# Optimization experiments

Measured on AMD Instinct MI355X. Metric: run time of the kernel, lower is better.

Reference implementation:

```python
import jax, jax.numpy as jnp
import numpy as np

MARKET_DIM, VELOCITY_DIM, AGENT_STATE_DIM = 20, 10, 10
RUNNER_DIM, POSITION_DIM, MAX_RUNNERS = 24, 8, 30
RUNNER_INPUT_DIM = RUNNER_DIM + POSITION_DIM            # 32
MARKET_TOTAL_DIM = MARKET_DIM + VELOCITY_DIM + AGENT_STATE_DIM  # 40
OBS_DIM = MARKET_DIM + VELOCITY_DIM + MAX_RUNNERS * RUNNER_DIM + AGENT_STATE_DIM + MAX_RUNNERS * POSITION_DIM  # 1000
TD_IDX = MARKET_DIM + (VELOCITY_DIM - 4)                # 26
B, T = 256, 64
MLP_H, LSTM_H = 128, 256
LSTM_IN = MLP_H + 2 * MLP_H                             # 384


def setup_inputs() -> dict:
    key = jax.random.key(0)
    ks = jax.random.split(key, 32)

    def w(k, o, i):
        return (jax.random.normal(k, (o, i), jnp.float32) / np.sqrt(i)).astype(jnp.float32)

    z = lambda n: jnp.zeros((n,), jnp.float32)
    return dict(
        obs=jax.random.normal(ks[0], (B, T, OBS_DIM), jnp.float32),
        # runner encoder: 32 -> 128 -> 128 -> 128
        re_w0=w(ks[1], MLP_H, RUNNER_INPUT_DIM), re_b0=z(MLP_H),
        re_w1=w(ks[2], MLP_H, MLP_H), re_b1=z(MLP_H),
        re_w2=w(ks[3], MLP_H, MLP_H), re_b2=z(MLP_H),
        # market encoder: 40 -> 128 -> 128 -> 128
        me_w0=w(ks[4], MLP_H, MARKET_TOTAL_DIM), me_b0=z(MLP_H),
        me_w1=w(ks[5], MLP_H, MLP_H), me_b1=z(MLP_H),
        me_w2=w(ks[6], MLP_H, MLP_H), me_b2=z(MLP_H),
        # TimeLSTM cell (single layer)
        W_ih=w(ks[7], 4 * LSTM_H, LSTM_IN), b_ih=z(4 * LSTM_H),
        W_hh=w(ks[8], 4 * LSTM_H, LSTM_H),
        W_dt=jnp.zeros((LSTM_H,), jnp.float32),
        # actor head: 384 -> 128 -> 2
        a_w0=w(ks[9], MLP_H, MLP_H + LSTM_H), a_b0=z(MLP_H),
        a_w1=w(ks[10], 2, MLP_H) * 0.01, a_b1=z(2),
        # critic head: 256 -> 128 -> 1
        c_w0=w(ks[11], MLP_H, LSTM_H), c_b0=z(MLP_H),
        c_w1=w(ks[12], 1, MLP_H), c_b1=z(1),
        log_std=jnp.zeros((MAX_RUNNERS * 2,), jnp.float32),
    )


def _mlp3(x, w0, b0, w1, b1, w2, b2):
    x = jax.nn.relu(x @ w0.T + b0)
    x = jax.nn.relu(x @ w1.T + b1)
    return x @ w2.T + b2


def _mlp2(x, w0, b0, w1, b1):
    return jax.nn.relu(x @ w0.T + b0) @ w1.T + b1


def reference(obs,
              re_w0, re_b0, re_w1, re_b1, re_w2, re_b2,
              me_w0, me_b0, me_w1, me_b1, me_w2, me_b2,
              W_ih, b_ih, W_hh, W_dt,
              a_w0, a_b0, a_w1, a_b1,
              c_w0, c_b0, c_w1, c_b1,
              log_std):
    b, t, _ = obs.shape
    of = obs.reshape(b * t, -1)
    market = of[:, :MARKET_DIM]
    vel = of[:, MARKET_DIM:MARKET_DIM + VELOCITY_DIM]
    rs = MARKET_DIM + VELOCITY_DIM
    re_ = rs + MAX_RUNNERS * RUNNER_DIM
    runners = of[:, rs:re_].reshape(b * t, MAX_RUNNERS, RUNNER_DIM)
    agent = of[:, re_:re_ + AGENT_STATE_DIM]
    ps = re_ + AGENT_STATE_DIM
    pos = of[:, ps:ps + MAX_RUNNERS * POSITION_DIM].reshape(b * t, MAX_RUNNERS, POSITION_DIM)

    market_feats = jnp.concatenate([market, vel, agent], axis=-1)        # (BT, 40)
    runner_feats = jnp.concatenate([runners, pos], axis=-1)              # (BT, R, 32)

    market_emb = _mlp3(market_feats, me_w0, me_b0, me_w1, me_b1, me_w2, me_b2)  # (BT, 128)
    runner_embs = _mlp3(runner_feats, re_w0, re_b0, re_w1, re_b1, re_w2, re_b2)  # (BT, R, 128)
    r_mean = runner_embs.mean(axis=1)
    r_max = runner_embs.max(axis=1)

    lstm_in = jnp.concatenate([market_emb, r_mean, r_max], axis=-1).reshape(b, t, LSTM_IN)
    dt = of[:, TD_IDX].reshape(b, t)

    h0 = jnp.zeros((b, LSTM_H), obs.dtype)
    c0 = jnp.zeros_like(h0)

    def step(hc, xs):
        h, c = hc
        x, d = xs                                           # (B, 384), (B,)
        gates = x @ W_ih.T + b_ih + h @ W_hh.T              # (B, 4H)
        i, f, g, o = jnp.split(gates, 4, axis=-1)
        f = f + W_dt * d[:, None]                           # time-modulated forget gate
        i, f, o = jax.nn.sigmoid(i), jax.nn.sigmoid(f), jax.nn.sigmoid(o)
        g = jnp.tanh(g)
        c_new = f * c + i * g
        h_new = o * jnp.tanh(c_new)
        return (h_new, c_new), None

    (h, c), _ = jax.lax.scan(step, (h0, c0), (lstm_in.transpose(1, 0, 2), dt.T))
    lstm_out = h  # layer_norm disabled -> identity

    runner_last = runner_embs.reshape(b, t, MAX_RUNNERS, MLP_H)[:, -1]   # (B, R, 128)
    actor_in = jnp.concatenate(
        [runner_last, jnp.broadcast_to(lstm_out[:, None, :], (b, MAX_RUNNERS, LSTM_H))], axis=-1)
    action_mean = _mlp2(actor_in, a_w0, a_b0, a_w1, a_b1).reshape(b, MAX_RUNNERS * 2)
    action_log_std = jnp.broadcast_to(log_std, action_mean.shape)
    value = _mlp2(lstm_out, c_w0, c_b0, c_w1, c_b1)                      # (B, 1)
    return action_mean, action_log_std, value, h, c
```

## Files before the change

kernel.cpp:

```cpp
#include <hip/hip_runtime.h>
#include <hip/hip_bf16.h>
#include <math.h>

#define Bn 256
#define Tn 64
#define OBSD 1000
#define NR 30
#define HD 128
#define LH 256
#define LIN 384
#define TDI 26

#define AM_OFF 0
#define ALS_OFF 15360
#define V_OFF 30720
#define H_OFF 30976
#define C_OFF 96512

typedef unsigned short u16;
typedef short bf16x8 __attribute__((ext_vector_type(8)));
typedef float f32x4 __attribute__((ext_vector_type(4)));

__device__ __forceinline__ float sigm(float x){ return 1.f/(1.f+__expf(-x)); }
__device__ __forceinline__ float tanhfast(float x){
    float ax = fabsf(x);
    float e = __expf(2.f*ax);
    float t = 1.f - 2.f/(e+1.f);
    return copysignf(t, x);
}

__device__ __forceinline__ u16 f2b(float f){
    union { __hip_bfloat16 h; u16 u; } cv;
    cv.h = __float2bfloat16(f);
    return cv.u;
}

__device__ __forceinline__ bf16x8 ld_b128_sys(const u16* p){
    bf16x8 r;
    asm volatile("global_load_dwordx4 %0, %1, off sc0 sc1"
                 : "=v"(r) : "v"(p) : "memory");
    return r;
}
__device__ __forceinline__ void st_b16_sys(u16* p, unsigned v){
    asm volatile("global_store_short %0, %1, off sc0 sc1"
                 :: "v"(p), "v"(v) : "memory");
}

#define MFMA(a,b,c) __builtin_amdgcn_mfma_f32_16x16x32_bf16(a,b,c,0,0,0)

__global__ void k_pack(const float* __restrict__ src, u16* __restrict__ dst,
                       int N, int K, int Kpad)
{
    int t = blockIdx.x*256 + threadIdx.x;
    if (t >= N*Kpad) return;
    int j = t / Kpad, k = t - j*Kpad;
    float v = (k < K) ? src[j*K + k] : 0.f;
    int ntile = j>>4, jr = j&15, kc = k>>5, ko = k&31;
    int lane = ((ko>>3)<<4) | jr, elem = ko&7;
    int KC = Kpad>>5;
    dst[(size_t)(((ntile*KC + kc)*64) + lane)*8 + elem] = f2b(v);
}

__global__ void k_pack_gi(const float* __restrict__ src, u16* __restrict__ dst, int K)
{
    int KC = K >> 5;
    int t = blockIdx.x*256 + threadIdx.x;
    if (t >= 1024*K) return;
    int n = t / K, k = t - n*K;
    int nt = n>>4, jr = n&15;
    int jg = nt>>2, g = nt&3;
    float v = src[(size_t)(g*256 + jg*16 + jr)*K + k];
    int kc = k>>5, ko = k&31;
    int lane = ((ko>>3)<<4) | jr, e = ko&7;
    dst[(size_t)(((nt*KC + kc)*64) + lane)*8 + e] = f2b(v);
}

__global__ void k_dtv(const float* __restrict__ obs, float* __restrict__ dtv)
{
    int idx = blockIdx.x*256 + threadIdx.x;
    int b = idx >> 6, t = idx & 63;
    dtv[t*256 + b] = obs[(size_t)idx*OBSD + TDI];
}

__global__ __launch_bounds__(256) void k_embed(
    const float* __restrict__ obs,
    const u16* __restrict__ pw0, const float* __restrict__ re_b0,
    const u16* __restrict__ pw1, const float* __restrict__ re_b1,
    const u16* __restrict__ pw2, const float* __restrict__ re_b2,
    u16* __restrict__ li_bf, float* __restrict__ runner_last)
{
    __shared__ __align__(16) u16 xr[64*40];
    __shared__ __align__(16) u16 act1[64*136];
    __shared__ __align__(16) u16 act2[64*136];
    __shared__ float bs0[128], bs1[128], bs2[128];

    int blk = blockIdx.x, tid = threadIdx.x;
    int bt0 = blk*2;

    for (int idx=tid; idx<2048; idx+=256){
        int r = idx>>5, k = idx&31;
        int sb = r>>5, rr = r&31;
        const float* row = obs + (size_t)(bt0+sb)*OBSD;
        float v = 0.f;
        if (rr < 30) v = (k<24) ? row[30 + rr*24 + k] : row[760 + rr*8 + (k-24)];
        xr[r*40 + k] = f2b(v);
    }
    if (tid < 128){ bs0[tid]=re_b0[tid]; bs1[tid]=re_b1[tid]; bs2[tid]=re_b2[tid]; }
    __syncthreads();

    int lane = tid & 63, wv = tid >> 6;
    int lr = lane & 15, lk = lane >> 4;
    f32x4 zero = {0.f,0.f,0.f,0.f};

    f32x4 d[4][2];

    {
        bf16x8 a0[4];
        #pragma unroll
        for (int m=0;m<4;m++) a0[m] = *(const bf16x8*)(xr + (m*16+lr)*40 + lk*8);
        #pragma unroll
        for (int ns=0; ns<2; ns++){
            int n = 2*wv + ns;
            bf16x8 b = *(const bf16x8*)(pw0 + (size_t)(n*64 + lane)*8);
            #pragma unroll
            for (int m=0;m<4;m++) d[m][ns] = MFMA(a0[m], b, zero);
        }
    }
    #pragma unroll
    for (int m=0;m<4;m++)
        #pragma unroll
        for (int ns=0;ns<2;ns++){
            int col = (2*wv+ns)*16 + lr;
            float bias = bs0[col];
            #pragma unroll
            for (int r=0;r<4;r++)
                act1[(m*16+lk*4+r)*136 + col] = f2b(fmaxf(d[m][ns][r] + bias, 0.f));
        }
    __syncthreads();

    #pragma unroll
    for (int m=0;m<4;m++)
        #pragma unroll
        for (int ns=0;ns<2;ns++) d[m][ns] = zero;
    #pragma unroll
    for (int kc=0; kc<4; kc++){
        bf16x8 am[4];
        #pragma unroll
        for (int m=0;m<4;m++) am[m] = *(const bf16x8*)(act1 + (m*16+lr)*136 + kc*32 + lk*8);
        #pragma unroll
        for (int ns=0; ns<2; ns++){
            int n = 2*wv + ns;
            bf16x8 b = *(const bf16x8*)(pw1 + (size_t)((n*4 + kc)*64 + lane)*8);
            #pragma unroll
            for (int m=0;m<4;m++) d[m][ns] = MFMA(am[m], b, d[m][ns]);
        }
    }
    #pragma unroll
    for (int m=0;m<4;m++)
        #pragma unroll
        for (int ns=0;ns<2;ns++){
            int col = (2*wv+ns)*16 + lr;
            float bias = bs1[col];
            #pragma unroll
            for (int r=0;r<4;r++)
                act2[(m*16+lk*4+r)*136 + col] = f2b(fmaxf(d[m][ns][r] + bias, 0.f));
        }
    __syncthreads();

    #pragma unroll
    for (int m=0;m<4;m++)
        #pragma unroll
        for (int ns=0;ns<2;ns++) d[m][ns] = zero;
    #pragma unroll
    for (int kc=0; kc<4; kc++){
        bf16x8 am[4];
        #pragma unroll
        for (int m=0;m<4;m++) am[m] = *(const bf16x8*)(act2 + (m*16+lr)*136 + kc*32 + lk*8);
        #pragma unroll
        for (int ns=0; ns<2; ns++){
            int n = 2*wv + ns;
            bf16x8 b = *(const bf16x8*)(pw2 + (size_t)((n*4 + kc)*64 + lane)*8);
            #pragma unroll
            for (int m=0;m<4;m++) d[m][ns] = MFMA(am[m], b, d[m][ns]);
        }
    }

    u16* li0 = li_bf + (size_t)bt0*LIN;
    u16* li1 = li_bf + (size_t)(bt0+1)*LIN;
    bool last1 = (((bt0+1) & 63) == 63);
    int bb1 = (bt0+1) >> 6;

    #pragma unroll
    for (int ns=0; ns<2; ns++){
        int col = (2*wv+ns)*16 + lr;
        float bias = bs2[col];
        float vals[4][4];
        float s0=0.f, m0=-3.4e38f, s1=0.f, m1=-3.4e38f;
        #pragma unroll
        for (int m=0;m<4;m++)
            #pragma unroll
            for (int r=0;r<4;r++){
                int rw = m*16 + lk*4 + r;
                float v = d[m][ns][r] + bias;
                vals[m][r] = v;
                if (m < 2){
                    bool ok = rw < 30;
                    s0 += ok ? v : 0.f;
                    m0 = fmaxf(m0, ok ? v : -3.4e38f);
                } else {
                    bool ok = (rw-32) < 30;
                    s1 += ok ? v : 0.f;
                    m1 = fmaxf(m1, ok ? v : -3.4e38f);
                }
            }
        s0 += __shfl_xor(s0, 16); s0 += __shfl_xor(s0, 32);
        m0 = fmaxf(m0, __shfl_xor(m0, 16)); m0 = fmaxf(m0, __shfl_xor(m0, 32));
        s1 += __shfl_xor(s1, 16); s1 += __shfl_xor(s1, 32);
        m1 = fmaxf(m1, __shfl_xor(m1, 16)); m1 = fmaxf(m1, __shfl_xor(m1, 32));
        if (lk == 0){
            li0[128 + col] = f2b(s0 * (1.0f/30.0f));
            li0[256 + col] = f2b(m0);
        }
        if (lk == 1){
            li1[128 + col] = f2b(s1 * (1.0f/30.0f));
            li1[256 + col] = f2b(m1);
        }
        if (last1){
            #pragma unroll
            for (int m=2;m<4;m++)
                #pragma unroll
                for (int r=0;r<4;r++){
                    int rw = m*16 + lk*4 + r - 32;
                    if (rw < 30) runner_last[(size_t)bb1*3840 + rw*128 + col] = vals[m][r];
                }
        }
    }
}

__global__ __launch_bounds__(256) void k_market(
    const float* __restrict__ obs,
    const u16* __restrict__ pm0, const float* __restrict__ me_b0,
    const u16* __restrict__ pm1, const float* __restrict__ me_b1,
    const u16* __restrict__ pm2, const float* __restrict__ me_b2,
    u16* __restrict__ li_bf)
{
    __shared__ __align__(16) u16 xm[32*72];
    __shared__ __align__(16) u16 ma1[32*136];
    __shared__ __align__(16) u16 ma2[32*136];
    __shared__ float bs0[128], bs1[128], bs2[128];

    int bt0 = blockIdx.x*32, tid = threadIdx.x;
    for (int idx=tid; idx<2048; idx+=256){
        int r = idx>>6, k = idx&63;
        const float* row = obs + (size_t)(bt0+r)*OBSD;
        float v = 0.f;
        if (k < 30) v = row[k];
        else if (k < 40) v = row[720 + k];
        xm[r*72 + k] = f2b(v);
    }
    if (tid < 128){ bs0[tid]=me_b0[tid]; bs1[tid]=me_b1[tid]; bs2[tid]=me_b2[tid]; }
    __syncthreads();

    int lane = tid & 63, wv = tid >> 6;
    int lr = lane & 15, lk = lane >> 4;
    f32x4 zero = {0.f,0.f,0.f,0.f};
    f32x4 d[2][2];

    #pragma unroll
    for (int m=0;m<2;m++)
        #pragma unroll
        for (int ns=0;ns<2;ns++) d[m][ns] = zero;
    #pragma unroll
    for (int kc=0; kc<2; kc++){
        bf16x8 a0 = *(const bf16x8*)(xm + lr*72      + kc*32 + lk*8);
        bf16x8 a1 = *(const bf16x8*)(xm + (16+lr)*72 + kc*32 + lk*8);
        #pragma unroll
        for (int ns=0; ns<2; ns++){
            int n = 2*wv + ns;
            bf16x8 b = *(const bf16x8*)(pm0 + (size_t)((n*2 + kc)*64 + lane)*8);
            d[0][ns] = MFMA(a0, b, d[0][ns]);
            d[1][ns] = MFMA(a1, b, d[1][ns]);
        }
    }
    #pragma unroll
    for (int m=0;m<2;m++)
        #pragma unroll
        for (int ns=0;ns<2;ns++){
            int col = (2*wv+ns)*16 + lr;
            float bias = bs0[col];
            #pragma unroll
            for (int r=0;r<4;r++){
                int rw = m*16 + lk*4 + r;
                ma1[rw*136 + col] = f2b(fmaxf(d[m][ns][r] + bias, 0.f));
            }
        }
    __syncthreads();

    #pragma unroll
    for (int m=0;m<2;m++)
        #pragma unroll
        for (int ns=0;ns<2;ns++) d[m][ns] = zero;
    #pragma unroll
    for (int kc=0; kc<4; kc++){
        bf16x8 a0 = *(const bf16x8*)(ma1 + lr*136      + kc*32 + lk*8);
        bf16x8 a1 = *(const bf16x8*)(ma1 + (16+lr)*136 + kc*32 + lk*8);
        #pragma unroll
        for (int ns=0; ns<2; ns++){
            int n = 2*wv + ns;
            bf16x8 b = *(const bf16x8*)(pm1 + (size_t)((n*4 + kc)*64 + lane)*8);
            d[0][ns] = MFMA(a0, b, d[0][ns]);
            d[1][ns] = MFMA(a1, b, d[1][ns]);
        }
    }
    #pragma unroll
    for (int m=0;m<2;m++)
        #pragma unroll
        for (int ns=0;ns<2;ns++){
            int col = (2*wv+ns)*16 + lr;
            float bias = bs1[col];
            #pragma unroll
            for (int r=0;r<4;r++){
                int rw = m*16 + lk*4 + r;
                ma2[rw*136 + col] = f2b(fmaxf(d[m][ns][r] + bias, 0.f));
            }
        }
    __syncthreads();

    #pragma unroll
    for (int m=0;m<2;m++)
        #pragma unroll
        for (int ns=0;ns<2;ns++) d[m][ns] = zero;
    #pragma unroll
    for (int kc=0; kc<4; kc++){
        bf16x8 a0 = *(const bf16x8*)(ma2 + lr*136      + kc*32 + lk*8);
        bf16x8 a1 = *(const bf16x8*)(ma2 + (16+lr)*136 + kc*32 + lk*8);
        #pragma unroll
        for (int ns=0; ns<2; ns++){
            int n = 2*wv + ns;
            bf16x8 b = *(const bf16x8*)(pm2 + (size_t)((n*4 + kc)*64 + lane)*8);
            d[0][ns] = MFMA(a0, b, d[0][ns]);
            d[1][ns] = MFMA(a1, b, d[1][ns]);
        }
    }
    #pragma unroll
    for (int m=0;m<2;m++)
        #pragma unroll
        for (int ns=0;ns<2;ns++){
            int col = (2*wv+ns)*16 + lr;
            float bias = bs2[col];
            #pragma unroll
            for (int r=0;r<4;r++){
                int rw = m*16 + lk*4 + r;
                li_bf[(size_t)(bt0+rw)*LIN + col] = f2b(d[m][ns][r] + bias);
            }
        }
}

__global__ __launch_bounds__(256) void k_xw(
    const u16* __restrict__ A, const u16* __restrict__ pwih,
    const float* __restrict__ b_ih, float* __restrict__ xw)
{
    __shared__ __align__(16) u16 bsh[48*512];

    int tid = threadIdx.x;
    int lane = tid & 63, wv = tid >> 6;
    int lr = lane & 15, lk = lane >> 4;
    int r0 = blockIdx.x*128 + wv*32;

    bf16x8 a[2][12];
    #pragma unroll
    for (int m=0;m<2;m++)
        #pragma unroll
        for (int kc=0;kc<12;kc++)
            a[m][kc] = *(const bf16x8*)(A + (size_t)(r0+m*16+lr)*384 + kc*32 + lk*8);

    for (int jg=0; jg<16; jg++){
        {
            const bf16x8* src = (const bf16x8*)(pwih + (size_t)jg*48*512);
            bf16x8* dst = (bf16x8*)bsh;
            #pragma unroll
            for (int i=0;i<12;i++)
                dst[tid + i*256] = src[tid + i*256];
        }
        __syncthreads();

        f32x4 acc[2][4];
        #pragma unroll
        for (int g=0; g<4; g++){
            float bias = b_ih[g*256 + jg*16 + lr];
            f32x4 v = {bias,bias,bias,bias};
            acc[0][g]=v; acc[1][g]=v;
        }
        #pragma unroll
        for (int kc=0; kc<12; kc++){
            bf16x8 b0 = *(const bf16x8*)(bsh + (size_t)((0*12+kc)*64+lane)*8);
            bf16x8 b1 = *(const bf16x8*)(bsh + (size_t)((1*12+kc)*64+lane)*8);
            bf16x8 b2 = *(const bf16x8*)(bsh + (size_t)((2*12+kc)*64+lane)*8);
            bf16x8 b3 = *(const bf16x8*)(bsh + (size_t)((3*12+kc)*64+lane)*8);
            #pragma unroll
            for (int m=0;m<2;m++){
                acc[m][0] = MFMA(a[m][kc], b0, acc[m][0]);
                acc[m][1] = MFMA(a[m][kc], b1, acc[m][1]);
                acc[m][2] = MFMA(a[m][kc], b2, acc[m][2]);
                acc[m][3] = MFMA(a[m][kc], b3, acc[m][3]);
            }
        }
        #pragma unroll
        for (int m=0;m<2;m++)
            #pragma unroll
            for (int g=0;g<4;g++)
                #pragma unroll
                for (int r=0;r<4;r++)
                    xw[(size_t)(r0+m*16+lk*4+r)*1024 + (jg*4+g)*16 + lr] = acc[m][g][r];
        __syncthreads();
    }
}

__global__ __launch_bounds__(256,1) void k_lstm_pair(
    const float* __restrict__ xw, const u16* __restrict__ pwhh,
    const float* __restrict__ W_dt, const float* __restrict__ dtv,
    u16* __restrict__ hb0, u16* __restrict__ hb1,
    float* __restrict__ hout, float* __restrict__ cout,
    unsigned int* __restrict__ flags)
{
    int tid = threadIdx.x;
    int lane = tid & 63, wv = tid >> 6;
    int lr = lane & 15, lk = lane >> 4;
    int blk = blockIdx.x;
    int p = blk >> 1, hf = blk & 1;
    int bb0 = p*16;
    int jg0 = hf*8 + wv*2;

    bf16x8 bfr[2][4][8];
    #pragma unroll
    for (int jl=0;jl<2;jl++)
        #pragma unroll
        for (int g=0;g<4;g++)
            #pragma unroll
            for (int kc=0;kc<8;kc++)
                bfr[jl][g][kc] = *(const bf16x8*)(pwhh + (size_t)((((jg0+jl)*4+g)*8+kc)*64+lane)*8);

    float wdt0 = W_dt[jg0*16 + lr];
    float wdt1 = W_dt[(jg0+1)*16 + lr];

    float cst[2][4] = {{0.f,0.f,0.f,0.f},{0.f,0.f,0.f,0.f}};
    bf16x8 a[8];
    #pragma unroll
    for (int kc=0;kc<8;kc++) a[kc] = (bf16x8)(short)0;

    int bth = bb0 + lk*4;

    float xwn[2][4][4];
    #pragma unroll
    for (int jl=0;jl<2;jl++)
        #pragma unroll
        for (int g=0;g<4;g++)
            #pragma unroll
            for (int r=0;r<4;r++)
                xwn[jl][g][r] = xw[(size_t)((bth+r)*64)*1024 + ((jg0+jl)*4+g)*16 + lr];
    float4 dtn = *(const float4*)(dtv + bth);

    unsigned int* myflag   = &flags[blk*64];
    unsigned int* partflag = &flags[(blk^1)*64];

    for (int t=0; t<64; t++){
        asm volatile("s_waitcnt vmcnt(0)" ::: "memory");
        __builtin_amdgcn_sched_barrier(0);

        f32x4 acc[2][4];
        #pragma unroll
        for (int jl=0;jl<2;jl++)
            #pragma unroll
            for (int g=0;g<4;g++){
                f32x4 v;
                v[0]=xwn[jl][g][0]; v[1]=xwn[jl][g][1];
                v[2]=xwn[jl][g][2]; v[3]=xwn[jl][g][3];
                acc[jl][g] = v;
            }

        #pragma unroll
        for (int kc=0; kc<8; kc++){
            #pragma unroll
            for (int jl=0;jl<2;jl++){
                acc[jl][0] = MFMA(a[kc], bfr[jl][0][kc], acc[jl][0]);
                acc[jl][1] = MFMA(a[kc], bfr[jl][1][kc], acc[jl][1]);
                acc[jl][2] = MFMA(a[kc], bfr[jl][2][kc], acc[jl][2]);
                acc[jl][3] = MFMA(a[kc], bfr[jl][3][kc], acc[jl][3]);
            }
        }

        u16* hw = (t&1) ? hb1 : hb0;
        #pragma unroll
        for (int jl=0;jl<2;jl++){
            float wdt = jl ? wdt1 : wdt0;
            int jcol = (jg0+jl)*16 + lr;
            #pragma unroll
            for (int r=0;r<4;r++){
                float dd = (r==0)?dtn.x:(r==1)?dtn.y:(r==2)?dtn.z:dtn.w;
                float gi = sigm(acc[jl][0][r]);
                float gf = sigm(acc[jl][1][r] + wdt*dd);
                float gg = tanhfast(acc[jl][2][r]);
                float go = sigm(acc[jl][3][r]);
                float cn = fmaf(gf, cst[jl][r], gi*gg);
                cst[jl][r] = cn;
                float hv = go * tanhfast(cn);
                if (t < 63){
                    st_b16_sys(hw + (size_t)(bth+r)*256 + jcol, (unsigned)f2b(hv));
                } else {
                    hout[(size_t)(bth+r)*256 + jcol] = hv;
                    cout[(size_t)(bth+r)*256 + jcol] = cn;
                }
            }
        }

        if (t < 63){
            asm volatile("s_waitcnt vmcnt(0)" ::: "memory");
            __syncthreads();
            if (tid == 0)
                __hip_atomic_store(myflag, (unsigned)(t+1),
                                   __ATOMIC_RELAXED, __HIP_MEMORY_SCOPE_SYSTEM);

            #pragma unroll
            for (int jl=0;jl<2;jl++)
                #pragma unroll
                for (int g=0;g<4;g++)
                    #pragma unroll
                    for (int r=0;r<4;r++)
                        xwn[jl][g][r] = xw[(size_t)((bth+r)*64 + (t+1))*1024 + ((jg0+jl)*4+g)*16 + lr];
            dtn = *(const float4*)(dtv + (t+1)*256 + bth);

            if (lane == 0){
                while (__hip_atomic_load(partflag, __ATOMIC_RELAXED,
                                         __HIP_MEMORY_SCOPE_SYSTEM) < (unsigned)(t+1)) {}
            }
            __builtin_amdgcn_wave_barrier();

            const u16* hr = (t&1) ? hb1 : hb0;
            #pragma unroll
            for (int kc=0; kc<8; kc++)
                a[kc] = ld_b128_sys(hr + (size_t)(bb0+lr)*256 + kc*32 + lk*8);
        }
    }
}

__device__ __forceinline__ void dense30(
    const float* in, int istride,
    const float* __restrict__ W, int wstride, int K,
    const float* __restrict__ bias, const float* extra,
    float* outp, int ostride, bool relu, int j, int rh)
{
    float acc[15];
    #pragma unroll
    for (int i=0;i<15;i++) acc[i]=0.f;
    const float* w = W + j*wstride;
    for (int k=0;k<K;k+=4){
        float4 wv = *(const float4*)(w+k);
        #pragma unroll
        for (int i=0;i<15;i++){
            float4 xv = *(const float4*)(in + (rh+2*i)*istride + k);
            acc[i] = fmaf(wv.x,xv.x,acc[i]);
            acc[i] = fmaf(wv.y,xv.y,acc[i]);
            acc[i] = fmaf(wv.z,xv.z,acc[i]);
            acc[i] = fmaf(wv.w,xv.w,acc[i]);
        }
    }
    float bb = bias[j] + (extra ? extra[j] : 0.f);
    #pragma unroll
    for (int i=0;i<15;i++){
        float v = acc[i]+bb;
        outp[(rh+2*i)*ostride+j] = relu ? fmaxf(v,0.f) : v;
    }
}

__device__ __forceinline__ float dense1(
    const float* in, const float* __restrict__ W,
    const float* __restrict__ bias, int K, int j)
{
    const float* w = W + j*K;
    float s = 0.f;
    for (int k=0;k<K;k+=4){
        float4 wv = *(const float4*)(w+k);
        float4 xv = *(const float4*)(in+k);
        s = fmaf(wv.x,xv.x,s); s = fmaf(wv.y,xv.y,s);
        s = fmaf(wv.z,xv.z,s); s = fmaf(wv.w,xv.w,s);
    }
    return s + bias[j];
}

__global__ __launch_bounds__(256) void k_heads(
    const float* __restrict__ h, const float* __restrict__ cbuf,
    const float* __restrict__ rl,
    const float* __restrict__ a_w0, const float* __restrict__ a_b0,
    const float* __restrict__ a_w1, const float* __restrict__ a_b1,
    const float* __restrict__ c_w0, const float* __restrict__ c_b0,
    const float* __restrict__ c_w1, const float* __restrict__ c_b1,
    const float* __restrict__ log_std,
    float* __restrict__ out)
{
    __shared__ __align__(16) float hv[LH];
    __shared__ __align__(16) float rls[NR][HD];
    __shared__ __align__(16) float hid[NR][HD];
    __shared__ __align__(16) float dot2[HD];
    __shared__ __align__(16) float red[128];

    int b = blockIdx.x, tid = threadIdx.x;
    hv[tid] = h[b*LH + tid];
    for (int idx=tid; idx<NR*HD; idx+=256) rls[idx>>7][idx&127] = rl[(size_t)b*NR*HD + idx];
    __syncthreads();

    if (tid < 128){
        const float* w = a_w0 + tid*LIN + HD;
        float s = 0.f;
        for (int k=0;k<LH;k+=4){
            float4 wv = *(const float4*)(w+k);
            s = fmaf(wv.x,hv[k],s); s = fmaf(wv.y,hv[k+1],s);
            s = fmaf(wv.z,hv[k+2],s); s = fmaf(wv.w,hv[k+3],s);
        }
        dot2[tid] = s;
    }
    __syncthreads();

    int j = tid & 127, rh = tid >> 7;
    dense30(&rls[0][0], HD, a_w0, LIN, HD, a_b0, dot2, &hid[0][0], HD, true, j, rh);
    __syncthreads();

    if (tid < 60){
        int r = tid >> 1, o = tid & 1;
        const float* w = a_w1 + o*HD;
        float s = a_b1[o];
        for (int k=0;k<HD;k++) s = fmaf(hid[r][k], w[k], s);
        out[AM_OFF + b*60 + tid] = s;
        out[ALS_OFF + b*60 + tid] = log_std[tid];
    }

    float term = 0.f;
    if (tid < 128) term = fmaxf(dense1(hv, c_w0, c_b0, LH, tid), 0.f) * c_w1[tid];
    if (tid < 128) red[tid] = term;
    __syncthreads();
    for (int s2=64; s2>0; s2>>=1){
        if (tid < s2) red[tid] += red[tid+s2];
        __syncthreads();
    }
    if (tid == 0) out[V_OFF + b] = red[0] + c_b1[0];

    out[H_OFF + b*LH + tid] = hv[tid];
    out[C_OFF + b*LH + tid] = cbuf[b*LH + tid];
}

extern "C" void kernel_launch(void* const* d_in, const int* in_sizes, int n_in,
                              void* d_out, int out_size, void* d_ws, size_t ws_size,
                              hipStream_t stream)
{
    const float* obs   = (const float*)d_in[0];
    const float* re_w0 = (const float*)d_in[1];
    const float* re_b0 = (const float*)d_in[2];
    const float* re_w1 = (const float*)d_in[3];
    const float* re_b1 = (const float*)d_in[4];
    const float* re_w2 = (const float*)d_in[5];
    const float* re_b2 = (const float*)d_in[6];
    const float* me_w0 = (const float*)d_in[7];
    const float* me_b0 = (const float*)d_in[8];
    const float* me_w1 = (const float*)d_in[9];
    const float* me_b1 = (const float*)d_in[10];
    const float* me_w2 = (const float*)d_in[11];
    const float* me_b2 = (const float*)d_in[12];
    const float* W_ih  = (const float*)d_in[13];
    const float* b_ih  = (const float*)d_in[14];
    const float* W_hh  = (const float*)d_in[15];
    const float* W_dt  = (const float*)d_in[16];
    const float* a_w0  = (const float*)d_in[17];
    const float* a_b0  = (const float*)d_in[18];
    const float* a_w1  = (const float*)d_in[19];
    const float* a_b1  = (const float*)d_in[20];
    const float* c_w0  = (const float*)d_in[21];
    const float* c_b0  = (const float*)d_in[22];
    const float* c_w1  = (const float*)d_in[23];
    const float* c_b1  = (const float*)d_in[24];
    const float* lstd  = (const float*)d_in[25];
    float* out = (float*)d_out;

    float* ws = (float*)d_ws;
    size_t off = 0;
    float* xw4  = ws + off; off += (size_t)16384*1024;
    float* hout = ws + off; off += (size_t)Bn*LH;
    float* cb   = ws + off; off += (size_t)Bn*LH;
    float* rl   = ws + off; off += (size_t)Bn*NR*HD;
    float* dtv  = ws + off; off += (size_t)16384;
    unsigned int* flags = (unsigned int*)(ws + off); off += 2048;

    u16* us = (u16*)(ws + off);
    size_t uo = 0;
    u16* li_bf = us + uo; uo += (size_t)16384*LIN;
    u16* pw0   = us + uo; uo += 128*32;
    u16* pw1   = us + uo; uo += 128*128;
    u16* pw2   = us + uo; uo += 128*128;
    u16* pm0   = us + uo; uo += 128*64;
    u16* pm1   = us + uo; uo += 128*128;
    u16* pm2   = us + uo; uo += 128*128;
    u16* pwih  = us + uo; uo += (size_t)1024*384;
    u16* pwhh  = us + uo; uo += (size_t)1024*256;
    u16* hb0   = us + uo; uo += (size_t)Bn*LH;
    u16* hb1   = us + uo; uo += (size_t)Bn*LH;

    hipMemsetAsync(flags, 0, 2048*sizeof(unsigned int), stream);

    k_pack<<<16,   256, 0, stream>>>(re_w0, pw0, 128, 32, 32);
    k_pack<<<64,   256, 0, stream>>>(re_w1, pw1, 128, 128, 128);
    k_pack<<<64,   256, 0, stream>>>(re_w2, pw2, 128, 128, 128);
    k_pack<<<32,   256, 0, stream>>>(me_w0, pm0, 128, 40, 64);
    k_pack<<<64,   256, 0, stream>>>(me_w1, pm1, 128, 128, 128);
    k_pack<<<64,   256, 0, stream>>>(me_w2, pm2, 128, 128, 128);
    k_pack_gi<<<1536, 256, 0, stream>>>(W_ih, pwih, 384);
    k_pack_gi<<<1024, 256, 0, stream>>>(W_hh, pwhh, 256);
    k_dtv<<<64, 256, 0, stream>>>(obs, dtv);

    k_embed<<<8192, 256, 0, stream>>>(obs, pw0, re_b0, pw1, re_b1, pw2, re_b2,
                                      li_bf, rl);
    k_market<<<512, 256, 0, stream>>>(obs, pm0, me_b0, pm1, me_b1, pm2, me_b2,
                                      li_bf);
    k_xw<<<128, 256, 0, stream>>>(li_bf, pwih, b_ih, xw4);

    k_lstm_pair<<<32, 256, 0, stream>>>(xw4, pwhh, W_dt, dtv, hb0, hb1,
                                        hout, cb, flags);

    k_heads<<<256, 256, 0, stream>>>(hout, cb, rl,
        a_w0, a_b0, a_w1, a_b1, c_w0, c_b0, c_w1, c_b1, lstd, out);
}
```

Baseline: 515.2 us.

## Split LSTM recurrent matmul so own-half K chunks run before partner sync

Each block of a pair now loads the half of h it wrote itself right after publishing its flag. It runs the MFMAs for those K chunks while the partner block is still finishing, and only after spinning on the partner flag does it load and multiply the remaining half. This moves half the recurrent matmul off the critical path of the inter-block handshake. A template parameter selects which half, at the cost of duplicated code and an extra vmcnt wait before the early MFMAs.

```diff
diff --git a/kernel.cpp b/kernel.cpp
--- a/kernel.cpp
+++ b/kernel.cpp
@@ -416,20 +416,21 @@
     }
 }
 
-__global__ __launch_bounds__(256,1) void k_lstm_pair(
+template<int HF>
+__device__ __forceinline__ void lstm_run(
+    int tid, int p,
     const float* __restrict__ xw, const u16* __restrict__ pwhh,
     const float* __restrict__ W_dt, const float* __restrict__ dtv,
     u16* __restrict__ hb0, u16* __restrict__ hb1,
     float* __restrict__ hout, float* __restrict__ cout,
-    unsigned int* __restrict__ flags)
-{
-    int tid = threadIdx.x;
+    unsigned int* myflag, unsigned int* partflag)
+{
     int lane = tid & 63, wv = tid >> 6;
     int lr = lane & 15, lk = lane >> 4;
-    int blk = blockIdx.x;
-    int p = blk >> 1, hf = blk & 1;
     int bb0 = p*16;
-    int jg0 = hf*8 + wv*2;
+    int jg0 = HF*8 + wv*2;
+    constexpr int OK0 = HF*4;
+    constexpr int PK0 = (1-HF)*4;
 
     bf16x8 bfr[2][4][8];
     #pragma unroll
@@ -460,32 +461,29 @@
                 xwn[jl][g][r] = xw[(size_t)((bth+r)*64)*1024 + ((jg0+jl)*4+g)*16 + lr];
     float4 dtn = *(const float4*)(dtv + bth);
 
-    unsigned int* myflag   = &flags[blk*64];
-    unsigned int* partflag = &flags[(blk^1)*64];
+    f32x4 acc[2][4];
+    #pragma unroll
+    for (int jl=0;jl<2;jl++)
+        #pragma unroll
+        for (int g=0;g<4;g++){
+            f32x4 v;
+            v[0]=xwn[jl][g][0]; v[1]=xwn[jl][g][1];
+            v[2]=xwn[jl][g][2]; v[3]=xwn[jl][g][3];
+            acc[jl][g] = v;
+        }
 
     for (int t=0; t<64; t++){
         asm volatile("s_waitcnt vmcnt(0)" ::: "memory");
         __builtin_amdgcn_sched_barrier(0);
 
-        f32x4 acc[2][4];
-        #pragma unroll
-        for (int jl=0;jl<2;jl++)
-            #pragma unroll
-            for (int g=0;g<4;g++){
-                f32x4 v;
-                v[0]=xwn[jl][g][0]; v[1]=xwn[jl][g][1];
-                v[2]=xwn[jl][g][2]; v[3]=xwn[jl][g][3];
-                acc[jl][g] = v;
-            }
-
-        #pragma unroll
-        for (int kc=0; kc<8; kc++){
+        #pragma unroll
+        for (int i=0;i<4;i++){
             #pragma unroll
             for (int jl=0;jl<2;jl++){
-                acc[jl][0] = MFMA(a[kc], bfr[jl][0][kc], acc[jl][0]);
-                acc[jl][1] = MFMA(a[kc], bfr[jl][1][kc], acc[jl][1]);
-                acc[jl][2] = MFMA(a[kc], bfr[jl][2][kc], acc[jl][2]);
-                acc[jl][3] = MFMA(a[kc], bfr[jl][3][kc], acc[jl][3]);
+                acc[jl][0] = MFMA(a[PK0+i], bfr[jl][0][PK0+i], acc[jl][0]);
+                acc[jl][1] = MFMA(a[PK0+i], bfr[jl][1][PK0+i], acc[jl][1]);
+                acc[jl][2] = MFMA(a[PK0+i], bfr[jl][2][PK0+i], acc[jl][2]);
+                acc[jl][3] = MFMA(a[PK0+i], bfr[jl][3][PK0+i], acc[jl][3]);
             }
         }
 
@@ -520,6 +518,12 @@
                 __hip_atomic_store(myflag, (unsigned)(t+1),
                                    __ATOMIC_RELAXED, __HIP_MEMORY_SCOPE_SYSTEM);
 
+            const u16* hr = (t&1) ? hb1 : hb0;
+
+            #pragma unroll
+            for (int i=0;i<4;i++)
+                a[OK0+i] = ld_b128_sys(hr + (size_t)(bb0+lr)*256 + (OK0+i)*32 + lk*8);
+
             #pragma unroll
             for (int jl=0;jl<2;jl++)
                 #pragma unroll
@@ -529,18 +533,60 @@
                         xwn[jl][g][r] = xw[(size_t)((bth+r)*64 + (t+1))*1024 + ((jg0+jl)*4+g)*16 + lr];
             dtn = *(const float4*)(dtv + (t+1)*256 + bth);
 
+            asm volatile("s_waitcnt vmcnt(0)" ::: "memory");
+            __builtin_amdgcn_sched_barrier(0);
+
+            #pragma unroll
+            for (int jl=0;jl<2;jl++)
+                #pragma unroll
+                for (int g=0;g<4;g++){
+                    f32x4 v;
+                    v[0]=xwn[jl][g][0]; v[1]=xwn[jl][g][1];
+                    v[2]=xwn[jl][g][2]; v[3]=xwn[jl][g][3];
+                    acc[jl][g] = v;
+                }
+            #pragma unroll
+            for (int i=0;i<4;i++){
+                #pragma unroll
+                for (int jl=0;jl<2;jl++){
+                    acc[jl][0] = MFMA(a[OK0+i], bfr[jl][0][OK0+i], acc[jl][0]);
+                    acc[jl][1] = MFMA(a[OK0+i], bfr[jl][1][OK0+i], acc[jl][1]);
+                    acc[jl][2] = MFMA(a[OK0+i], bfr[jl][2][OK0+i], acc[jl][2]);
+                    acc[jl][3] = MFMA(a[OK0+i], bfr[jl][3][OK0+i], acc[jl][3]);
+                }
+            }
+
             if (lane == 0){
                 while (__hip_atomic_load(partflag, __ATOMIC_RELAXED,
                                          __HIP_MEMORY_SCOPE_SYSTEM) < (unsigned)(t+1)) {}
             }
             __builtin_amdgcn_wave_barrier();
 
-            const u16* hr = (t&1) ? hb1 : hb0;
-            #pragma unroll
-            for (int kc=0; kc<8; kc++)
-                a[kc] = ld_b128_sys(hr + (size_t)(bb0+lr)*256 + kc*32 + lk*8);
-        }
-    }
+            #pragma unroll
+            for (int i=0;i<4;i++)
+                a[PK0+i] = ld_b128_sys(hr + (size_t)(bb0+lr)*256 + (PK0+i)*32 + lk*8);
+        }
+    }
+}
+
+__global__ __launch_bounds__(256,1) void k_lstm_pair(
+    const float* __restrict__ xw, const u16* __restrict__ pwhh,
+    const float* __restrict__ W_dt, const float* __restrict__ dtv,
+    u16* __restrict__ hb0, u16* __restrict__ hb1,
+    float* __restrict__ hout, float* __restrict__ cout,
+    unsigned int* __restrict__ flags)
+{
+    int blk = blockIdx.x;
+    int p = blk >> 1, hf = blk & 1;
+    unsigned int* myflag   = &flags[blk*64];
+    unsigned int* partflag = &flags[(blk^1)*64];
+
+    if (hf == 0)
+        lstm_run<0>(threadIdx.x, p, xw, pwhh, W_dt, dtv, hb0, hb1, hout, cout,
+                    myflag, partflag);
+    else
+        lstm_run<1>(threadIdx.x, p, xw, pwhh, W_dt, dtv, hb0, hb1, hout, cout,
+                    myflag, partflag);
 }
 
 __device__ __forceinline__ void dense30(
```

Result: slower. 527.5 us (+2.4%).
